# Kernel optimization log

Hardware: AMD Instinct MI355X
Metric: run time of the kernel (lower is better)

The kernel has to match this reference:

```python
import jax, jax.numpy as jnp
import numpy as np

KS = 63      # Gaussian kernel size (module default)
SIGMA = 32.0 # Gaussian sigma (module default)


def _gaussian_kernel2d(k, sigma):
    # kornia get_gaussian_kernel2d: outer product of normalized 1D gaussians
    x = jnp.arange(k, dtype=jnp.float32) - k // 2
    g = jnp.exp(-(x * x) / (2.0 * sigma * sigma))
    g = g / g.sum()
    return jnp.outer(g, g)  # [k,k]


def _filter2d_constant(x, k2d):
    # kornia filter2d, border_type='constant' (zero pad), depthwise per channel
    C = x.shape[1]
    kern = jnp.broadcast_to(k2d, (C, 1) + k2d.shape)  # [C,1,k,k]
    return jax.lax.conv_general_dilated(
        x, kern, window_strides=(1, 1), padding='SAME',
        dimension_numbers=('NCHW', 'OIHW', 'NCHW'), feature_group_count=C)


def _grid_sample_bilinear(img, grid, align_corners=False):
    # torch.nn.functional.grid_sample, mode='bilinear', padding_mode='zeros'
    B, C, H, W = img.shape
    gx, gy = grid[..., 0], grid[..., 1]
    if align_corners:
        x = (gx + 1.0) * (W - 1) * 0.5
        y = (gy + 1.0) * (H - 1) * 0.5
    else:
        x = ((gx + 1.0) * W - 1.0) * 0.5
        y = ((gy + 1.0) * H - 1.0) * 0.5
    x0 = jnp.floor(x); y0 = jnp.floor(y)
    x0i = x0.astype(jnp.int32); y0i = y0.astype(jnp.int32)
    x1i = x0i + 1; y1i = y0i + 1
    wx1 = x - x0; wx0 = 1.0 - wx1
    wy1 = y - y0; wy0 = 1.0 - wy1

    def gather(iy, ix):
        valid = ((ix >= 0) & (ix < W) & (iy >= 0) & (iy < H))
        iyc = jnp.clip(iy, 0, H - 1)
        ixc = jnp.clip(ix, 0, W - 1)
        # per-batch fancy gather: [B,C,H,W]
        v = jax.vmap(lambda im, yy, xx: im[:, yy, xx])(img, iyc, ixc)
        return v * valid[:, None].astype(img.dtype)

    out = (gather(y0i, x0i) * (wy0 * wx0)[:, None]
           + gather(y0i, x1i) * (wy0 * wx1)[:, None]
           + gather(y1i, x0i) * (wy1 * wx0)[:, None]
           + gather(y1i, x1i) * (wy1 * wx1)[:, None])
    return out


def setup_inputs() -> dict:
    key = jax.random.key(0)
    k1, k2 = jax.random.split(key)
    image = jax.random.normal(k1, (8, 3, 512, 512), dtype=jnp.float32)
    noise = jax.random.uniform(k2, (8, 2, 512, 512), dtype=jnp.float32)
    return {"image": image, "noise": noise}


def reference(image, noise):
    B, C, H, W = image.shape
    noise = noise * 2.0 - 1.0                      # rand*2-1 as in forward()
    k2d = _gaussian_kernel2d(KS, SIGMA)
    disp_xy = _filter2d_constant(noise, k2d)       # [B,2,H,W]
    disp = jnp.transpose(disp_xy, (0, 2, 3, 1))    # [B,H,W,2] (x,y)
    # kornia create_meshgrid(normalized_coordinates=True): linspace(-1,1)
    xs = jnp.linspace(-1.0, 1.0, W, dtype=image.dtype)
    ys = jnp.linspace(-1.0, 1.0, H, dtype=image.dtype)
    base = jnp.stack(jnp.meshgrid(xs, ys, indexing='xy'), axis=-1)  # [H,W,2]
    grid = jnp.clip(base[None] + disp, -1.0, 1.0)
    warped = _grid_sample_bilinear(image, grid, align_corners=False)
    return warped, disp
```

## Files before the change

kernel.cpp:

```cpp
#include <hip/hip_runtime.h>
#include <math.h>

#define KS 63
#define RAD 31
#define NB 8
#define NC 3
#define NH 512
#define NW 512
#define PADH 576

struct GaussW { float w[KS]; };

__global__ __launch_bounds__(256) void hblur_kernel(const float* __restrict__ noise,
                                                    float* __restrict__ tmp, GaussW gw) {
    const int bid = blockIdx.x;
    const int t = threadIdx.x;
    if (bid >= NB * NH) {
        const int pid = bid - NB * NH;
        const int img = pid >> 5;
        const int pr  = pid & 31;
        const int row = (pr < 16) ? (pr * 2) : (544 + (pr - 16) * 2);
        float4* dst = (float4*)(tmp + ((size_t)img * PADH + row) * NW);
        dst[t] = make_float4(0.f, 0.f, 0.f, 0.f);
        return;
    }
    const int b = bid >> 9;
    const int h = bid & (NH - 1);
    const int ch = t >> 7;
    const int tt = t & 127;

    __shared__ float rows[2][PADH];
    const float* src = noise + ((size_t)(b * 2 + ch) * NH + h) * NW;
    {
        const float4 nv = *(const float4*)(src + 4 * tt);
        float4 sv;
        sv.x = fmaf(nv.x, 2.f, -1.f); sv.y = fmaf(nv.y, 2.f, -1.f);
        sv.z = fmaf(nv.z, 2.f, -1.f); sv.w = fmaf(nv.w, 2.f, -1.f);
        *(float4*)&rows[ch][32 + 4 * tt] = sv;
        if (tt < 8) {
            *(float4*)&rows[ch][4 * tt]       = make_float4(0.f, 0.f, 0.f, 0.f);
            *(float4*)&rows[ch][544 + 4 * tt] = make_float4(0.f, 0.f, 0.f, 0.f);
        }
    }
    __syncthreads();

    float acc[4] = {0.f, 0.f, 0.f, 0.f};
#pragma unroll
    for (int c = 0; c < 17; ++c) {
        const float4 v = *(const float4*)&rows[ch][4 * tt + 4 * c];
        const float vv[4] = {v.x, v.y, v.z, v.w};
#pragma unroll
        for (int e = 0; e < 4; ++e) {
#pragma unroll
            for (int oo = 0; oo < 4; ++oo) {
                const int j = 4 * c + e - oo - 1;
                if (j >= 0 && j < KS) acc[oo] = fmaf(vv[e], gw.w[j], acc[oo]);
            }
        }
    }
    float4* dst = (float4*)(tmp + (((size_t)(b * 2 + ch) * PADH) + 32 + h) * NW + 4 * tt);
    *dst = make_float4(acc[0], acc[1], acc[2], acc[3]);
}

__global__ __launch_bounds__(256) void vblur_kernel(const float* __restrict__ tmp,
                                                    float2* __restrict__ disp, GaussW gw) {
    const int t = threadIdx.x;
    const int bid = blockIdx.x;
    const int wt = bid & 1;
    const int ht = (bid >> 1) & 63;
    const int b  = bid >> 7;
    const int w  = wt * 256 + t;
    const int h0 = ht * 8;

    const float* c0 = tmp + (((size_t)(b * 2 + 0) * PADH) + h0 + 1) * NW + w;
    const float* c1 = tmp + (((size_t)(b * 2 + 1) * PADH) + h0 + 1) * NW + w;

    float ax[8] = {0,0,0,0,0,0,0,0};
    float ay[8] = {0,0,0,0,0,0,0,0};
#pragma unroll
    for (int rr = 0; rr < 70; ++rr) {
        const float vx = c0[(size_t)rr * NW];
        const float vy = c1[(size_t)rr * NW];
#pragma unroll
        for (int o = 0; o < 8; ++o) {
            const int j = rr - o;
            if (j >= 0 && j < KS) {
                ax[o] = fmaf(vx, gw.w[j], ax[o]);
                ay[o] = fmaf(vy, gw.w[j], ay[o]);
            }
        }
    }
#pragma unroll
    for (int o = 0; o < 8; ++o)
        disp[((size_t)b * NH + h0 + o) * NW + w] = make_float2(ax[o], ay[o]);
}

__global__ __launch_bounds__(256) void warp_kernel(const float* __restrict__ img,
                                                   const float2* __restrict__ disp,
                                                   float* __restrict__ warped) {
    const int idx = blockIdx.x * 256 + threadIdx.x;
    const int w = idx & (NW - 1);
    const int h = (idx >> 9) & (NH - 1);
    const int b = idx >> 18;
    const float2 d = disp[idx];

    float gx = fmaf((float)w, 2.0f / 511.0f, -1.0f) + d.x;
    float gy = fmaf((float)h, 2.0f / 511.0f, -1.0f) + d.y;
    gx = fminf(1.f, fmaxf(-1.f, gx));
    gy = fminf(1.f, fmaxf(-1.f, gy));

    const float x = ((gx + 1.0f) * (float)NW - 1.0f) * 0.5f;
    const float y = ((gy + 1.0f) * (float)NH - 1.0f) * 0.5f;
    const float xf = floorf(x), yf = floorf(y);
    const int x0 = (int)xf, y0 = (int)yf;
    const int x1 = x0 + 1,  y1 = y0 + 1;
    const float wx1 = x - xf, wx0 = 1.0f - wx1;
    const float wy1 = y - yf, wy0 = 1.0f - wy1;
    const bool vx0 = ((unsigned)x0 < NW), vx1 = ((unsigned)x1 < NW);
    const bool vy0 = ((unsigned)y0 < NH), vy1 = ((unsigned)y1 < NH);
    const int x0c = min(max(x0, 0), NW - 1), x1c = min(max(x1, 0), NW - 1);
    const int y0c = min(max(y0, 0), NH - 1), y1c = min(max(y1, 0), NH - 1);
    const float w00 = wy0 * wx0, w01 = wy0 * wx1;
    const float w10 = wy1 * wx0, w11 = wy1 * wx1;

    const size_t base = (size_t)b * NC * NH * NW;
    const size_t o00 = (size_t)y0c * NW + x0c, o01 = (size_t)y0c * NW + x1c;
    const size_t o10 = (size_t)y1c * NW + x0c, o11 = (size_t)y1c * NW + x1c;
#pragma unroll
    for (int c = 0; c < NC; ++c) {
        const float* ic = img + base + (size_t)c * NH * NW;
        const float v00 = (vy0 && vx0) ? ic[o00] : 0.f;
        const float v01 = (vy0 && vx1) ? ic[o01] : 0.f;
        const float v10 = (vy1 && vx0) ? ic[o10] : 0.f;
        const float v11 = (vy1 && vx1) ? ic[o11] : 0.f;
        const float r = ((v00 * w00 + v01 * w01) + v10 * w10) + v11 * w11;
        warped[base + (size_t)c * NH * NW + (size_t)h * NW + w] = r;
    }
}

extern "C" void kernel_launch(void* const* d_in, const int* in_sizes, int n_in,
                              void* d_out, int out_size, void* d_ws, size_t ws_size,
                              hipStream_t stream) {
    const float* image = (const float*)d_in[0];
    const float* noise = (const float*)d_in[1];
    float* warped = (float*)d_out;
    float* dispo  = (float*)d_out + (size_t)NB * NC * NH * NW;

    GaussW gw;
    float s = 0.f;
    for (int i = 0; i < KS; ++i) {
        const float xv = (float)(i - RAD);
        gw.w[i] = expf(-(xv * xv) / (2.0f * 32.0f * 32.0f));
        s += gw.w[i];
    }
    for (int i = 0; i < KS; ++i) gw.w[i] /= s;

    float* scratch = warped;

    hblur_kernel<<<NB * NH + 512, 256, 0, stream>>>(noise, scratch, gw);
    vblur_kernel<<<NB * (NH / 8) * 2, 256, 0, stream>>>(scratch, (float2*)dispo, gw);
    warp_kernel<<<(NB * NH * NW) / 256, 256, 0, stream>>>(image, (const float2*)dispo, warped);
}
```

Baseline: 142.2 us.

## Fuse vertical blur with bilinear warp and move scratch to workspace

Merges the vertical blur and warp kernels, so each thread computes eight displacement values and immediately performs the bilinear sampling for those pixels. This removes one launch and the reread of the displacement buffer. The scratch buffer moves from the warped output to the workspace, which is needed because the fused kernel writes warped while tmp is still being read. Validity masks become weight multipliers and the loads are unconditional (clamped), which adds register pressure and leaves fewer blocks to hide gather latency.

```diff
diff --git a/kernel.cpp b/kernel.cpp
--- a/kernel.cpp
+++ b/kernel.cpp
@@ -62,8 +62,11 @@
     *dst = make_float4(acc[0], acc[1], acc[2], acc[3]);
 }
 
-__global__ __launch_bounds__(256) void vblur_kernel(const float* __restrict__ tmp,
-                                                    float2* __restrict__ disp, GaussW gw) {
+__global__ __launch_bounds__(256) void vwarp_kernel(const float* __restrict__ tmp,
+                                                    const float* __restrict__ img,
+                                                    float2* __restrict__ disp,
+                                                    float* __restrict__ warped,
+                                                    GaussW gw) {
     const int t = threadIdx.x;
     const int bid = blockIdx.x;
     const int wt = bid & 1;
@@ -90,51 +93,44 @@
             }
         }
     }
+
+    const float gxb = fmaf((float)w, 2.0f / 511.0f, -1.0f);
+    const float* i0 = img + (size_t)b * NC * NH * NW;
+    const float* i1 = i0 + NH * NW;
+    const float* i2 = i1 + NH * NW;
+    float* wp = warped + (size_t)b * NC * NH * NW;
+
 #pragma unroll
-    for (int o = 0; o < 8; ++o)
-        disp[((size_t)b * NH + h0 + o) * NW + w] = make_float2(ax[o], ay[o]);
-}
+    for (int o = 0; o < 8; ++o) {
+        const int h = h0 + o;
+        disp[((size_t)b * NH + h) * NW + w] = make_float2(ax[o], ay[o]);
 
-__global__ __launch_bounds__(256) void warp_kernel(const float* __restrict__ img,
-                                                   const float2* __restrict__ disp,
-                                                   float* __restrict__ warped) {
-    const int idx = blockIdx.x * 256 + threadIdx.x;
-    const int w = idx & (NW - 1);
-    const int h = (idx >> 9) & (NH - 1);
-    const int b = idx >> 18;
-    const float2 d = disp[idx];
+        float gx = gxb + ax[o];
+        float gy = fmaf((float)h, 2.0f / 511.0f, -1.0f) + ay[o];
+        gx = fminf(1.f, fmaxf(-1.f, gx));
+        gy = fminf(1.f, fmaxf(-1.f, gy));
 
-    float gx = fmaf((float)w, 2.0f / 511.0f, -1.0f) + d.x;
-    float gy = fmaf((float)h, 2.0f / 511.0f, -1.0f) + d.y;
-    gx = fminf(1.f, fmaxf(-1.f, gx));
-    gy = fminf(1.f, fmaxf(-1.f, gy));
-
-    const float x = ((gx + 1.0f) * (float)NW - 1.0f) * 0.5f;
-    const float y = ((gy + 1.0f) * (float)NH - 1.0f) * 0.5f;
-    const float xf = floorf(x), yf = floorf(y);
-    const int x0 = (int)xf, y0 = (int)yf;
-    const int x1 = x0 + 1,  y1 = y0 + 1;
-    const float wx1 = x - xf, wx0 = 1.0f - wx1;
-    const float wy1 = y - yf, wy0 = 1.0f - wy1;
-    const bool vx0 = ((unsigned)x0 < NW), vx1 = ((unsigned)x1 < NW);
-    const bool vy0 = ((unsigned)y0 < NH), vy1 = ((unsigned)y1 < NH);
-    const int x0c = min(max(x0, 0), NW - 1), x1c = min(max(x1, 0), NW - 1);
-    const int y0c = min(max(y0, 0), NH - 1), y1c = min(max(y1, 0), NH - 1);
-    const float w00 = wy0 * wx0, w01 = wy0 * wx1;
-    const float w10 = wy1 * wx0, w11 = wy1 * wx1;
-
-    const size_t base = (size_t)b * NC * NH * NW;
-    const size_t o00 = (size_t)y0c * NW + x0c, o01 = (size_t)y0c * NW + x1c;
-    const size_t o10 = (size_t)y1c * NW + x0c, o11 = (size_t)y1c * NW + x1c;
-#pragma unroll
-    for (int c = 0; c < NC; ++c) {
-        const float* ic = img + base + (size_t)c * NH * NW;
-        const float v00 = (vy0 && vx0) ? ic[o00] : 0.f;
-        const float v01 = (vy0 && vx1) ? ic[o01] : 0.f;
-        const float v10 = (vy1 && vx0) ? ic[o10] : 0.f;
-        const float v11 = (vy1 && vx1) ? ic[o11] : 0.f;
-        const float r = ((v00 * w00 + v01 * w01) + v10 * w10) + v11 * w11;
-        warped[base + (size_t)c * NH * NW + (size_t)h * NW + w] = r;
+        const float x = ((gx + 1.0f) * (float)NW - 1.0f) * 0.5f;
+        const float y = ((gy + 1.0f) * (float)NH - 1.0f) * 0.5f;
+        const float xf = floorf(x), yf = floorf(y);
+        const int x0 = (int)xf, y0 = (int)yf;
+        const int x1 = x0 + 1,  y1 = y0 + 1;
+        const float wx1 = x - xf, wx0 = 1.0f - wx1;
+        const float wy1 = y - yf, wy0 = 1.0f - wy1;
+        const float fx0 = ((unsigned)x0 < NW) ? 1.f : 0.f;
+        const float fx1 = ((unsigned)x1 < NW) ? 1.f : 0.f;
+        const float fy0 = ((unsigned)y0 < NH) ? 1.f : 0.f;
+        const float fy1 = ((unsigned)y1 < NH) ? 1.f : 0.f;
+        const int x0c = min(max(x0, 0), NW - 1), x1c = min(max(x1, 0), NW - 1);
+        const int y0c = min(max(y0, 0), NH - 1), y1c = min(max(y1, 0), NH - 1);
+        const float w00 = wy0 * wx0 * (fy0 * fx0), w01 = wy0 * wx1 * (fy0 * fx1);
+        const float w10 = wy1 * wx0 * (fy1 * fx0), w11 = wy1 * wx1 * (fy1 * fx1);
+        const int o00 = y0c * NW + x0c, o01 = y0c * NW + x1c;
+        const int o10 = y1c * NW + x0c, o11 = y1c * NW + x1c;
+        const size_t po = (size_t)h * NW + w;
+        wp[po]               = ((i0[o00] * w00 + i0[o01] * w01) + i0[o10] * w10) + i0[o11] * w11;
+        wp[NH * NW + po]     = ((i1[o00] * w00 + i1[o01] * w01) + i1[o10] * w10) + i1[o11] * w11;
+        wp[2 * NH * NW + po] = ((i2[o00] * w00 + i2[o01] * w01) + i2[o10] * w10) + i2[o11] * w11;
     }
 }
 
@@ -145,6 +141,7 @@
     const float* noise = (const float*)d_in[1];
     float* warped = (float*)d_out;
     float* dispo  = (float*)d_out + (size_t)NB * NC * NH * NW;
+    float* scratch = (float*)d_ws;
 
     GaussW gw;
     float s = 0.f;
@@ -155,9 +152,7 @@
     }
     for (int i = 0; i < KS; ++i) gw.w[i] /= s;
 
-    float* scratch = warped;
-
     hblur_kernel<<<NB * NH + 512, 256, 0, stream>>>(noise, scratch, gw);
-    vblur_kernel<<<NB * (NH / 8) * 2, 256, 0, stream>>>(scratch, (float2*)dispo, gw);
-    warp_kernel<<<(NB * NH * NW) / 256, 256, 0, stream>>>(image, (const float2*)dispo, warped);
+    vwarp_kernel<<<NB * (NH / 8) * 2, 256, 0, stream>>>(scratch, image,
+                                                        (float2*)dispo, warped, gw);
 }
```

Result: faster. 136.4 us (median of 2 runs) (-4.0%).
